# Optimization experiments

Hardware: AMD Instinct MI355X
Metric: run time of the kernel (lower is better)

The kernel has to match this reference:

```python
import jax, jax.numpy as jnp
import numpy as np

V, D = 100000, 300          # vocab, embedding dim
B, L, T, C, I = 64, 256, 1, 10, 6  # batch, positions, targets, context, info samples


def setup_inputs() -> dict:
    key = jax.random.key(0)
    ks = jax.random.split(key, 8)
    # indices start at 1 so padding_idx=0 (zero row, no grad in torch) never appears
    pos_u = jax.random.randint(ks[0], (B, L, T), 1, V)
    pos_v = jax.random.randint(ks[1], (B, L, C), 1, V)
    info_v = jax.random.randint(ks[2], (B, L, I), 1, V)
    initrange = 1.0 / D
    W_out = jax.random.uniform(ks[3], (V, D), minval=-initrange, maxval=initrange, dtype=jnp.float32)
    # torch inits W_in to 0; use a small random init so the baseline is non-degenerate
    W_in = jax.random.uniform(ks[4], (V, D), minval=-initrange, maxval=initrange, dtype=jnp.float32)
    W_out = W_out.at[0].set(0.0)
    W_in = W_in.at[0].set(0.0)
    context_mask = (jax.random.uniform(ks[5], (C,)) > 0.2).astype(jnp.float32)
    sig_mask = jnp.where(jax.random.uniform(ks[6], (I,)) > 0.5, 1.0, -1.0).astype(jnp.float32)
    score_mask = jax.random.uniform(ks[7], (I,), dtype=jnp.float32)
    return {"pos_u": pos_u, "pos_v": pos_v, "info_v": info_v,
            "W_in": W_in, "W_out": W_out,
            "context_mask": context_mask, "sig_mask": sig_mask, "score_mask": score_mask}


def reference(pos_u, pos_v, info_v, W_in, W_out, context_mask, sig_mask, score_mask):
    tgt_out = W_out[pos_u]    # [B,L,T,D]
    ctx_in = W_in[pos_v]      # [B,L,C,D]
    ctx_out = W_out[pos_v]    # [B,L,C,D]
    info_in = W_in[info_v]    # [B,L,I,D]
    # dropout disabled (p=0, eval-mode determinism)
    ctx_in = ctx_in * context_mask[None, None, :, None]
    # target-context scores: [B,L,T,C]
    score = jnp.einsum('bltd,blcd->bltc', tgt_out, ctx_in)
    score = jnp.clip(score, -10.0, 10.0)
    loss = -jnp.sum(jax.nn.log_sigmoid(score))
    # context-info scores: [B,L,C,I]
    info_score = jnp.einsum('blcd,blid->blci', ctx_out, info_in)
    info_score = jnp.clip(info_score, -10.0, 10.0)
    info_score = info_score * sig_mask          # sign flip for negative samples
    info_score = -jax.nn.log_sigmoid(info_score) * score_mask
    return loss + jnp.sum(info_score)
```

## Files before the change

### kernel.cpp

```cpp
#include <hip/hip_runtime.h>

#define D_ 300
#define C_ 10
#define I_ 6
#define NPOS 16384
#define PPB 4
#define NBLK (NPOS / PPB)
#define CHUNK 35

__device__ __forceinline__ float neg_log_sigmoid(float x) {
    return __logf(1.0f + __expf(-x));
}

__global__ __launch_bounds__(256, 4) void hg2vec_pos_kernel(
    const int* __restrict__ pos_u, const int* __restrict__ pos_v,
    const int* __restrict__ info_v,
    const float* __restrict__ W_in, const float* __restrict__ W_out,
    const float* __restrict__ context_mask, const float* __restrict__ sig_mask,
    const float* __restrict__ score_mask, float* __restrict__ partial)
{
    const int wave = threadIdx.x >> 6;
    const int lane = threadIdx.x & 63;
    const int p = blockIdx.x * PPB + wave;

    __shared__ float s_red[PPB][CHUNK][65];
    __shared__ float s_wsum[PPB];

    const int su = __builtin_amdgcn_readfirstlane(pos_u[p]);
    int scv[C_], siv[I_];
#pragma unroll
    for (int c = 0; c < C_; ++c) scv[c] = __builtin_amdgcn_readfirstlane(pos_v[p * C_ + c]);
#pragma unroll
    for (int i = 0; i < I_; ++i) siv[i] = __builtin_amdgcn_readfirstlane(info_v[p * I_ + i]);

    const int k4 = lane + 256;
    const float okf = (k4 < D_) ? 1.0f : 0.0f;
    const int k4c = (k4 < D_) ? k4 : lane;

    const float* ur = W_out + (size_t)su * D_;
    float u0 = ur[lane], u1 = ur[lane + 64], u2 = ur[lane + 128], u3 = ur[lane + 192];
    float u4 = ur[k4c] * okf;

    float ii0[I_], ii1[I_], ii2[I_], ii3[I_], ii4[I_];
#pragma unroll
    for (int i = 0; i < I_; ++i) {
        const float* r = W_in + (size_t)siv[i] * D_;
        ii0[i] = r[lane];       ii1[i] = r[lane + 64];
        ii2[i] = r[lane + 128]; ii3[i] = r[lane + 192];
        ii4[i] = r[k4c] * okf;
    }

    float acc = 0.0f;

#pragma unroll
    for (int chunk = 0; chunk < 2; ++chunk) {
        float part[CHUNK];
#pragma unroll
        for (int cc = 0; cc < 5; ++cc) {
            const int c = chunk * 5 + cc;
            const float* cir = W_in  + (size_t)scv[c] * D_;
            const float* cor = W_out + (size_t)scv[c] * D_;
            float a0 = cir[lane], a1 = cir[lane + 64], a2 = cir[lane + 128],
                  a3 = cir[lane + 192], a4 = cir[k4c];
            float b0 = cor[lane], b1 = cor[lane + 64], b2 = cor[lane + 128],
                  b3 = cor[lane + 192], b4 = cor[k4c];
            part[cc * 7] = u0 * a0 + u1 * a1 + u2 * a2 + u3 * a3 + u4 * a4;
#pragma unroll
            for (int i = 0; i < I_; ++i)
                part[cc * 7 + 1 + i] =
                    b0 * ii0[i] + b1 * ii1[i] + b2 * ii2[i] + b3 * ii3[i] + b4 * ii4[i];
        }

        __syncthreads();
#pragma unroll
        for (int d = 0; d < CHUNK; ++d) s_red[wave][d][lane] = part[d];
        __syncthreads();

        if (lane < CHUNK) {
            float s0 = 0, s1 = 0, s2 = 0, s3 = 0;
#pragma unroll
            for (int l = 0; l < 64; l += 4) {
                s0 += s_red[wave][lane][l + 0];
                s1 += s_red[wave][lane][l + 1];
                s2 += s_red[wave][lane][l + 2];
                s3 += s_red[wave][lane][l + 3];
            }
            float dot = (s0 + s1) + (s2 + s3);
            const int cc = lane / 7;
            const int t  = lane - cc * 7;
            const int c  = chunk * 5 + cc;
            float term;
            if (t == 0) {
                float x = dot * context_mask[c];
                x = fminf(fmaxf(x, -10.0f), 10.0f);
                term = neg_log_sigmoid(x);
            } else {
                const int i = t - 1;
                float x = fminf(fmaxf(dot, -10.0f), 10.0f) * sig_mask[i];
                term = neg_log_sigmoid(x) * score_mask[i];
            }
            acc += term;
        }
    }

#pragma unroll
    for (int off = 32; off; off >>= 1) acc += __shfl_xor(acc, off, 64);
    if (lane == 0) s_wsum[wave] = acc;
    __syncthreads();
    if (threadIdx.x == 0)
        partial[blockIdx.x] = s_wsum[0] + s_wsum[1] + s_wsum[2] + s_wsum[3];
}

__global__ __launch_bounds__(1024) void hg2vec_reduce_kernel(
    const float* __restrict__ partial, float* __restrict__ out)
{
    float4 v = ((const float4*)partial)[threadIdx.x];
    float a = (v.x + v.y) + (v.z + v.w);
#pragma unroll
    for (int off = 32; off; off >>= 1) a += __shfl_xor(a, off, 64);
    __shared__ float s[16];
    if ((threadIdx.x & 63) == 0) s[threadIdx.x >> 6] = a;
    __syncthreads();
    if (threadIdx.x == 0) {
        float t = 0;
#pragma unroll
        for (int i = 0; i < 16; ++i) t += s[i];
        out[0] = t;
    }
}

extern "C" void kernel_launch(void* const* d_in, const int* in_sizes, int n_in,
                              void* d_out, int out_size, void* d_ws, size_t ws_size,
                              hipStream_t stream) {
    const int* pos_u = (const int*)d_in[0];
    const int* pos_v = (const int*)d_in[1];
    const int* info_v = (const int*)d_in[2];
    const float* W_in = (const float*)d_in[3];
    const float* W_out = (const float*)d_in[4];
    const float* context_mask = (const float*)d_in[5];
    const float* sig_mask = (const float*)d_in[6];
    const float* score_mask = (const float*)d_in[7];
    float* out = (float*)d_out;
    float* partial = (float*)d_ws;

    hg2vec_pos_kernel<<<NBLK, 256, 0, stream>>>(
        pos_u, pos_v, info_v, W_in, W_out,
        context_mask, sig_mask, score_mask, partial);
    hg2vec_reduce_kernel<<<1, 1024, 0, stream>>>(partial, out);
}
```

Baseline: 286.0 us.

## Vectorize row loads to float4 and pre-reduce partial dots with lane shuffles

Embedding rows are now read as float4 per lane (columns 0-255) plus one scalar tail, instead of four strided scalar loads. Each partial dot is folded across groups of 4 lanes with xor shuffles before going to shared memory. This shrinks the LDS staging buffer to 16 entries per dot and removes the two-chunk loop and one barrier pair. Launch bounds rise to 8 waves per SIMD to raise occupancy. The cost is many extra shuffle instructions and more register pressure, which could cause spills under the new bound.

```diff
diff --git a/kernel.cpp b/kernel.cpp
--- a/kernel.cpp
+++ b/kernel.cpp
@@ -6,13 +6,14 @@
 #define NPOS 16384
 #define PPB 4
 #define NBLK (NPOS / PPB)
-#define CHUNK 35
+#define NDOT 70
+#define NGRP 16
 
 __device__ __forceinline__ float neg_log_sigmoid(float x) {
     return __logf(1.0f + __expf(-x));
 }
 
-__global__ __launch_bounds__(256, 4) void hg2vec_pos_kernel(
+__global__ __launch_bounds__(256, 8) void hg2vec_pos_kernel(
     const int* __restrict__ pos_u, const int* __restrict__ pos_v,
     const int* __restrict__ info_v,
     const float* __restrict__ W_in, const float* __restrict__ W_out,
@@ -22,73 +23,75 @@
     const int wave = threadIdx.x >> 6;
     const int lane = threadIdx.x & 63;
     const int p = blockIdx.x * PPB + wave;
+    const int sp = __builtin_amdgcn_readfirstlane(p);
 
-    __shared__ float s_red[PPB][CHUNK][65];
+    __shared__ float s_red[PPB][NDOT][NGRP + 1];
     __shared__ float s_wsum[PPB];
 
-    const int su = __builtin_amdgcn_readfirstlane(pos_u[p]);
+    const int su = pos_u[sp];
     int scv[C_], siv[I_];
 #pragma unroll
-    for (int c = 0; c < C_; ++c) scv[c] = __builtin_amdgcn_readfirstlane(pos_v[p * C_ + c]);
+    for (int c = 0; c < C_; ++c) scv[c] = pos_v[sp * C_ + c];
 #pragma unroll
-    for (int i = 0; i < I_; ++i) siv[i] = __builtin_amdgcn_readfirstlane(info_v[p * I_ + i]);
+    for (int i = 0; i < I_; ++i) siv[i] = info_v[sp * I_ + i];
 
     const int k4 = lane + 256;
     const float okf = (k4 < D_) ? 1.0f : 0.0f;
     const int k4c = (k4 < D_) ? k4 : lane;
 
     const float* ur = W_out + (size_t)su * D_;
-    float u0 = ur[lane], u1 = ur[lane + 64], u2 = ur[lane + 128], u3 = ur[lane + 192];
+    float4 uv = *(const float4*)(ur + 4 * lane);
     float u4 = ur[k4c] * okf;
 
-    float ii0[I_], ii1[I_], ii2[I_], ii3[I_], ii4[I_];
+    float4 iv[I_];
+    float it[I_];
 #pragma unroll
     for (int i = 0; i < I_; ++i) {
         const float* r = W_in + (size_t)siv[i] * D_;
-        ii0[i] = r[lane];       ii1[i] = r[lane + 64];
-        ii2[i] = r[lane + 128]; ii3[i] = r[lane + 192];
-        ii4[i] = r[k4c] * okf;
+        iv[i] = *(const float4*)(r + 4 * lane);
+        it[i] = r[k4c] * okf;
     }
 
-    float acc = 0.0f;
+#pragma unroll
+    for (int c = 0; c < C_; ++c) {
+        const float* cir = W_in  + (size_t)scv[c] * D_;
+        const float* cor = W_out + (size_t)scv[c] * D_;
+        float4 av = *(const float4*)(cir + 4 * lane);
+        float  a4 = cir[k4c];
+        float4 bv = *(const float4*)(cor + 4 * lane);
+        float  b4 = cor[k4c];
+
+        float pr[7];
+        pr[0] = uv.x * av.x + uv.y * av.y + uv.z * av.z + uv.w * av.w + u4 * a4;
+#pragma unroll
+        for (int i = 0; i < I_; ++i)
+            pr[1 + i] = bv.x * iv[i].x + bv.y * iv[i].y +
+                        bv.z * iv[i].z + bv.w * iv[i].w + b4 * it[i];
 
 #pragma unroll
-    for (int chunk = 0; chunk < 2; ++chunk) {
-        float part[CHUNK];
+        for (int t = 0; t < 7; ++t) {
+            float v = pr[t];
+            v += __shfl_xor(v, 1, 64);
+            v += __shfl_xor(v, 2, 64);
+            if ((lane & 3) == 0) s_red[wave][c * 7 + t][lane >> 2] = v;
+        }
+    }
+
+    __syncthreads();
+
+    float acc = 0.0f;
+    if (lane < 35) {
 #pragma unroll
-        for (int cc = 0; cc < 5; ++cc) {
-            const int c = chunk * 5 + cc;
-            const float* cir = W_in  + (size_t)scv[c] * D_;
-            const float* cor = W_out + (size_t)scv[c] * D_;
-            float a0 = cir[lane], a1 = cir[lane + 64], a2 = cir[lane + 128],
-                  a3 = cir[lane + 192], a4 = cir[k4c];
-            float b0 = cor[lane], b1 = cor[lane + 64], b2 = cor[lane + 128],
-                  b3 = cor[lane + 192], b4 = cor[k4c];
-            part[cc * 7] = u0 * a0 + u1 * a1 + u2 * a2 + u3 * a3 + u4 * a4;
-#pragma unroll
-            for (int i = 0; i < I_; ++i)
-                part[cc * 7 + 1 + i] =
-                    b0 * ii0[i] + b1 * ii1[i] + b2 * ii2[i] + b3 * ii3[i] + b4 * ii4[i];
-        }
-
-        __syncthreads();
-#pragma unroll
-        for (int d = 0; d < CHUNK; ++d) s_red[wave][d][lane] = part[d];
-        __syncthreads();
-
-        if (lane < CHUNK) {
-            float s0 = 0, s1 = 0, s2 = 0, s3 = 0;
-#pragma unroll
-            for (int l = 0; l < 64; l += 4) {
-                s0 += s_red[wave][lane][l + 0];
-                s1 += s_red[wave][lane][l + 1];
-                s2 += s_red[wave][lane][l + 2];
-                s3 += s_red[wave][lane][l + 3];
-            }
+        for (int rep = 0; rep < 2; ++rep) {
+            const int d = lane + rep * 35;
+            const float* rowp = s_red[wave][d];
+            float s0 = rowp[0] + rowp[4] + rowp[8]  + rowp[12];
+            float s1 = rowp[1] + rowp[5] + rowp[9]  + rowp[13];
+            float s2 = rowp[2] + rowp[6] + rowp[10] + rowp[14];
+            float s3 = rowp[3] + rowp[7] + rowp[11] + rowp[15];
             float dot = (s0 + s1) + (s2 + s3);
-            const int cc = lane / 7;
-            const int t  = lane - cc * 7;
-            const int c  = chunk * 5 + cc;
+            const int c = d / 7;
+            const int t = d - c * 7;
             float term;
             if (t == 0) {
                 float x = dot * context_mask[c];
```

Measured after the change: 289.0 us. About the same (+1.1%).
